# Kernel tuning notes

Hardware: AMD Instinct MI355X
Metric: run time of the kernel (lower is better)

## Reference

```python
import jax, jax.numpy as jnp
import numpy as np
import math

EMBED_DIM = 1024
N_HEAD = 16
HEAD_DIM = EMBED_DIM // N_HEAD


def setup_inputs() -> dict:
    key = jax.random.key(0)
    ks = jax.random.split(key, 9)
    B, T, C = 4, 2048, EMBED_DIM
    s = 1.0 / math.sqrt(C)
    return {
        "x": jax.random.normal(ks[0], (B, T, C), dtype=jnp.float32),
        "Wq": jax.random.normal(ks[1], (C, C), dtype=jnp.float32) * s,
        "bq": jnp.zeros((C,), dtype=jnp.float32),
        "Wk": jax.random.normal(ks[2], (C, C), dtype=jnp.float32) * s,
        "bk": jnp.zeros((C,), dtype=jnp.float32),
        "Wv": jax.random.normal(ks[3], (C, C), dtype=jnp.float32) * s,
        "bv": jnp.zeros((C,), dtype=jnp.float32),
        "Wp": jax.random.normal(ks[4], (C, C), dtype=jnp.float32) * s,
        "bp": jnp.zeros((C,), dtype=jnp.float32),
    }


def reference(x, Wq, bq, Wk, bk, Wv, bv, Wp, bp):
    B, T, C = x.shape
    H, D = N_HEAD, HEAD_DIM

    def heads(W, b):
        # [B,T,C] -> [B,H,T,D]
        return (x @ W.T + b).reshape(B, T, H, D).transpose(0, 2, 1, 3)

    q = heads(Wq, bq)
    k = heads(Wk, bk)
    v = heads(Wv, bv)

    att = jnp.einsum("bhtd,bhsd->bhts", q, k) * (1.0 / math.sqrt(D))
    causal = jnp.tril(jnp.ones((T, T), dtype=bool))
    att = jnp.where(causal[None, None], att, -jnp.inf)
    att = jax.nn.softmax(att, axis=-1)
    y = jnp.einsum("bhts,bhsd->bhtd", att, v)  # [B,H,T,D]
    y = y.transpose(0, 2, 1, 3).reshape(B, T, C)
    return y @ Wp.T + bp
```

## Files before the change

kernel.cpp:

```cpp
#include <hip/hip_runtime.h>
#include <hip/hip_bf16.h>
#include <cstdint>
#include <cstddef>

#define TQ 2048
#define CDIM 1024
#define NH 16
#define HD 64

typedef __attribute__((ext_vector_type(8))) short bf16x8;
typedef __attribute__((ext_vector_type(4))) float f32x4;
typedef __attribute__((ext_vector_type(16))) float f32x16;

__device__ __forceinline__ unsigned short f2bf(float f) {
  union { float f; unsigned u; } x; x.f = f;
  unsigned r = x.u + 0x7fffu + ((x.u >> 16) & 1u);
  return (unsigned short)(r >> 16);
}

__device__ __forceinline__ unsigned cvtpk(float lo, float hi) {
  unsigned r;
  asm("v_cvt_pk_bf16_f32 %0, %1, %2" : "=v"(r) : "v"(lo), "v"(hi));
  return r;
}

__device__ __forceinline__ void plswap(unsigned& x, unsigned& y) {
  asm("v_permlane32_swap_b32 %0, %1" : "+v"(x), "+v"(y));
}

__device__ __forceinline__ float exp2_fast(float x) {
  float r;
  asm("v_exp_f32 %0, %1" : "=v"(r) : "v"(x));
  return r;
}

__device__ __forceinline__ void gload_lds16(const void* g, void* l) {
  typedef __attribute__((address_space(1))) const void gv;
  typedef __attribute__((address_space(3))) void lv;
  __builtin_amdgcn_global_load_lds((gv*)g, (lv*)l, 16, 0, 0);
}

#define BAR() do { asm volatile("" ::: "memory"); __builtin_amdgcn_s_barrier(); asm volatile("" ::: "memory"); } while (0)
#define VMC2() asm volatile("s_waitcnt vmcnt(2)" ::: "memory")
#define VMC0() asm volatile("s_waitcnt vmcnt(0)" ::: "memory")

__global__ void cvt_bf16_kernel(const float* __restrict__ in,
                                unsigned short* __restrict__ out, int n) {
  int stride = gridDim.x * blockDim.x;
  for (int i = blockIdx.x * blockDim.x + threadIdx.x; i * 4 < n; i += stride) {
    float4 v = *(const float4*)(in + (size_t)i * 4);
    ushort4 o;
    o.x = f2bf(v.x); o.y = f2bf(v.y); o.z = f2bf(v.z); o.w = f2bf(v.w);
    *(ushort4*)(out + (size_t)i * 4) = o;
  }
}

__global__ void cvt4_kernel(const float* __restrict__ w0, const float* __restrict__ w1,
                            const float* __restrict__ w2, const float* __restrict__ w3,
                            unsigned short* __restrict__ out) {
  int i = blockIdx.x * blockDim.x + threadIdx.x;
  int which = i >> 18;
  const float* src = which == 0 ? w0 : which == 1 ? w1 : which == 2 ? w2 : w3;
  int off = (i & 262143) * 4;
  float4 v = *(const float4*)(src + off);
  ushort4 o;
  o.x = f2bf(v.x); o.y = f2bf(v.y); o.z = f2bf(v.z); o.w = f2bf(v.w);
  *(ushort4*)(out + (size_t)i * 4) = o;
}

template <int EPI>
__global__ __launch_bounds__(512, 2) void gemm128x256_kernel(
    const unsigned short* __restrict__ A,
    const unsigned short* __restrict__ Bt,
    const float* __restrict__ b0, const float* __restrict__ b1,
    void* __restrict__ outp,
    int M, int N, int K) {
  __shared__ __align__(16) char lds[98304];

  const int tid = (int)threadIdx.x;
  const int w = tid >> 6, lane = tid & 63;
  const int g = lane >> 4, c = lane & 15;
  const int wm = w >> 2, wn = w & 3;

  const int nbm = M >> 7, nbn = N >> 8;
  const int nwg = nbm * nbn;
  int id = (int)blockIdx.x;
  const int cpx = nwg >> 3;
  id = (id & 7) * cpx + (id >> 3);
  const int tm = id % nbm, tn = id / nbm;

  const char* Ab = (const char*)(A + (size_t)tm * 128 * K);
  const char* Bb = (const char*)(Bt + (size_t)tn * 256 * K);
  const int rowB = K * 2;
  const int nt = K >> 6;

  auto stageA = [&](int t) {
    if (t >= nt) return;
    char* dst = lds + (t & 1) * 49152 + (w << 11);
    const char* s = Ab + (size_t)(w * 16 + c) * rowB + t * 128 + g * 16;
    gload_lds16(s, dst);
    gload_lds16(s + 64, dst + 1024);
  };
  auto stageB = [&](int t, int odd) {
    if (t >= nt) return;
    const int n16 = (w >> 1) * 4 + 2 * odd + (w & 1);
    char* dst = lds + (t & 1) * 49152 + 16384 + (n16 << 11);
    const char* s = Bb + (size_t)(n16 * 16 + c) * rowB + t * 128 + g * 16;
    gload_lds16(s, dst);
    gload_lds16(s + 64, dst + 1024);
  };

  f32x4 acc[4][4];
#pragma unroll
  for (int i = 0; i < 4; ++i)
#pragma unroll
    for (int j = 0; j < 4; ++j) acc[i][j] = (f32x4){0.f, 0.f, 0.f, 0.f};
  bf16x8 af[2][2], bv[2][2][2];

  auto rdA = [&](int cur, int ms) {
#pragma unroll
    for (int mi2 = 0; mi2 < 2; ++mi2)
#pragma unroll
      for (int ki = 0; ki < 2; ++ki)
        af[mi2][ki] = *(const bf16x8*)(lds + cur * 49152 +
            (((wm * 4 + ms * 2 + mi2) << 1) + ki) * 1024 + lane * 16);
  };
  auto rdB = [&](int cur, int ns) {
#pragma unroll
    for (int ni2 = 0; ni2 < 2; ++ni2)
#pragma unroll
      for (int ki = 0; ki < 2; ++ki)
        bv[ns][ni2][ki] = *(const bf16x8*)(lds + cur * 49152 + 16384 +
            (((wn * 4 + ns * 2 + ni2) << 1) + ki) * 1024 + lane * 16);
  };
  auto mm = [&](int ms, int ns) {
    __builtin_amdgcn_s_setprio(1);
#pragma unroll
    for (int mi2 = 0; mi2 < 2; ++mi2)
#pragma unroll
      for (int ni2 = 0; ni2 < 2; ++ni2)
#pragma unroll
        for (int ki = 0; ki < 2; ++ki)
          acc[ms * 2 + mi2][ns * 2 + ni2] = __builtin_amdgcn_mfma_f32_16x16x32_bf16(
              af[mi2][ki], bv[ns][ni2][ki], acc[ms * 2 + mi2][ns * 2 + ni2], 0, 0, 0);
    __builtin_amdgcn_s_setprio(0);
  };

  stageA(0); stageB(0, 0); stageB(0, 1);
  VMC2();
  BAR();

#pragma unroll 1
  for (int i = 0; i < (nt >> 1); ++i) {
    const int t0 = 2 * i, t1 = 2 * i + 1;
    rdA(0, 0); rdB(0, 0); stageA(t0 + 1);
    mm(0, 0); VMC2(); BAR();
    rdB(0, 1); stageB(t0 + 1, 0);
    mm(0, 1); BAR();
    rdA(0, 1); stageB(t0 + 1, 1);
    mm(1, 1); BAR();
    mm(1, 0); VMC2(); BAR();
    rdA(1, 0); rdB(1, 0); stageA(t1 + 1);
    mm(0, 0);
    if (t1 == nt - 1) { VMC0(); } else { VMC2(); }
    BAR();
    rdB(1, 1); stageB(t1 + 1, 0);
    mm(0, 1); BAR();
    rdA(1, 1); stageB(t1 + 1, 1);
    mm(1, 1); BAR();
    mm(1, 0); VMC2(); BAR();
  }

#pragma unroll
  for (int mi = 0; mi < 4; ++mi) {
#pragma unroll
    for (int ni = 0; ni < 4; ++ni) {
      const int n = tn * 256 + wn * 64 + ni * 16 + c;
#pragma unroll
      for (int e = 0; e < 4; ++e) {
        const int m = tm * 128 + wm * 64 + mi * 16 + g * 4 + e;
        float v = acc[mi][ni][e];
        if (EPI == 1) {
          v += b0[m];
          size_t idx = ((size_t)(n >> 11) * (NH * HD) + m) * TQ + (n & (TQ - 1));
          ((unsigned short*)outp)[idx] = f2bf(v);
        } else if (EPI == 2) {
          v += b0[n];
          ((float*)outp)[(size_t)m * N + n] = v;
        } else {
          unsigned short* O = (unsigned short*)outp;
          if (n < 1024) {
            v = (v + b0[n]) * 0.18033688f;
            size_t idx = ((size_t)(m >> 11) * NH + (n >> 6)) * (TQ * HD) +
                         (size_t)(m & (TQ - 1)) * HD + (n & (HD - 1));
            O[idx] = f2bf(v);
          } else {
            int nn = n - 1024;
            v += b1[nn];
            size_t idx = 8388608 + ((size_t)(m >> 11) * NH + (nn >> 6)) * (TQ * HD) +
                         (size_t)(m & (TQ - 1)) * HD + (nn & (HD - 1));
            O[idx] = f2bf(v);
          }
        }
      }
    }
  }
}

__global__ __launch_bounds__(256, 4) void attn_kernel(
    const unsigned short* __restrict__ Q,
    const unsigned short* __restrict__ K,
    const unsigned short* __restrict__ Vt,
    unsigned short* __restrict__ Y) {
  __shared__ __align__(16) char Ks[2][8192];
  __shared__ __align__(16) char Vs[2][8192];

  const int tid = (int)threadIdx.x;
  const int w = tid >> 6, lane = tid & 63;
  const int l31 = lane & 31, hi = lane >> 5;

  const int n = (int)blockIdx.x;
  const int g = n & 255, k = n >> 8;
  const int bh = g >> 2;
  const int u = 2 * (g & 3) + (k >> 1);
  const int qt = (k & 1) ? (15 - u) : u;
  const int b = bh >> 4, h = bh & 15;

  const unsigned short* Qb = Q + (size_t)bh * TQ * HD;
  const char* Kb = (const char*)(K + (size_t)bh * TQ * HD);
  const char* Vb = (const char*)(Vt + (size_t)bh * HD * TQ);

  auto stage = [&](int buf, int kt) {
#pragma unroll
    for (int i = 0; i < 2; ++i) {
      const int s = i * 256 + tid;
      const int r32 = (s >> 8) * 32 + (s & 31);
      const int ck = ((s >> 6) & 3) * 32 + ((s >> 5) & 1) * 16;
      char* kdst = &Ks[buf][0] + i * 4096 + (w << 10);
      char* vdst = &Vs[buf][0] + i * 4096 + (w << 10);
      gload_lds16(Kb + (size_t)kt * 8192 + r32 * 128 + ck, kdst);
      gload_lds16(Vb + (size_t)r32 * 4096 + kt * 128 + ck, vdst);
    }
  };

  const int q0 = qt * 128 + w * 32;
  const int qg = q0 + l31;
  const int nkv = 2 * qt + 2;

  stage(0, 0);

  bf16x8 qf[4];
#pragma unroll
  for (int dk = 0; dk < 4; ++dk)
    qf[dk] = *(const bf16x8*)(Qb + (size_t)qg * HD + dk * 16 + hi * 8);

  f32x16 oac[2];
#pragma unroll
  for (int nb = 0; nb < 2; ++nb)
#pragma unroll
    for (int r = 0; r < 16; ++r) oac[nb][r] = 0.f;
  float mr = -3.0e38f, lr = 0.f;

  __syncthreads();

  for (int kt = 0; kt < nkv; ++kt) {
    const int cur = kt & 1;
    if (kt + 1 < nkv) stage(cur ^ 1, kt + 1);

    if (kt * 64 <= q0 + 31) {
      const char* Klane = &Ks[cur][0] + lane * 16;
      const char* Vlane = &Vs[cur][0] + lane * 16;

      f32x16 s0, s1;
#pragma unroll
      for (int r = 0; r < 16; ++r) { s0[r] = 0.f; s1[r] = 0.f; }
#pragma unroll
      for (int dk = 0; dk < 4; ++dk) {
        bf16x8 kf0 = *(const bf16x8*)(Klane + (dk << 10));
        bf16x8 kf1 = *(const bf16x8*)(Klane + ((4 + dk) << 10));
        s0 = __builtin_amdgcn_mfma_f32_32x32x16_bf16(kf0, qf[dk], s0, 0, 0, 0);
        s1 = __builtin_amdgcn_mfma_f32_32x32x16_bf16(kf1, qf[dk], s1, 0, 0, 0);
      }

      const bool maskT = (kt * 64 + 63 > q0);
      if (maskT) {
#pragma unroll
        for (int r = 0; r < 16; ++r) {
          int kv0 = kt * 64 + ((r & 3) + 8 * (r >> 2)) + 4 * hi;
          s0[r] = (kv0 <= qg) ? s0[r] : -3.0e38f;
          s1[r] = (kv0 + 32 <= qg) ? s1[r] : -3.0e38f;
        }
      }

      float mt_ = s0[0];
#pragma unroll
      for (int r = 1; r < 16; ++r) mt_ = fmaxf(mt_, s0[r]);
#pragma unroll
      for (int r = 0; r < 16; ++r) mt_ = fmaxf(mt_, s1[r]);
      mt_ = fmaxf(mt_, __shfl_xor(mt_, 32));

      if (!__all(mt_ - mr <= 8.0f)) {
        const float mn = fmaxf(mr, mt_);
        const float al = exp2_fast(mr - mn);
        mr = mn;
        lr *= al;
#pragma unroll
        for (int nb = 0; nb < 2; ++nb)
#pragma unroll
          for (int r = 0; r < 16; ++r) oac[nb][r] *= al;
      }

      float rs = 0.f;
#pragma unroll
      for (int r = 0; r < 16; ++r) { s0[r] = exp2_fast(s0[r] - mr); rs += s0[r]; }
#pragma unroll
      for (int r = 0; r < 16; ++r) { s1[r] = exp2_fast(s1[r] - mr); rs += s1[r]; }
      rs += __shfl_xor(rs, 32);
      lr += rs;

      bf16x8 pf[4];
      {
        unsigned a0 = cvtpk(s0[0], s0[1]), b0 = cvtpk(s0[2], s0[3]);
        unsigned c0 = cvtpk(s0[4], s0[5]), d0 = cvtpk(s0[6], s0[7]);
        plswap(a0, c0); plswap(b0, d0);
        unsigned a1 = cvtpk(s0[8], s0[9]), b1 = cvtpk(s0[10], s0[11]);
        unsigned c1 = cvtpk(s0[12], s0[13]), d1 = cvtpk(s0[14], s0[15]);
        plswap(a1, c1); plswap(b1, d1);
        unsigned a2 = cvtpk(s1[0], s1[1]), b2 = cvtpk(s1[2], s1[3]);
        unsigned c2 = cvtpk(s1[4], s1[5]), d2 = cvtpk(s1[6], s1[7]);
        plswap(a2, c2); plswap(b2, d2);
        unsigned a3 = cvtpk(s1[8], s1[9]), b3 = cvtpk(s1[10], s1[11]);
        unsigned c3 = cvtpk(s1[12], s1[13]), d3 = cvtpk(s1[14], s1[15]);
        plswap(a3, c3); plswap(b3, d3);
        union { unsigned u[4]; bf16x8 v; } t;
        t.u[0] = a0; t.u[1] = b0; t.u[2] = c0; t.u[3] = d0; pf[0] = t.v;
        t.u[0] = a1; t.u[1] = b1; t.u[2] = c1; t.u[3] = d1; pf[1] = t.v;
        t.u[0] = a2; t.u[1] = b2; t.u[2] = c2; t.u[3] = d2; pf[2] = t.v;
        t.u[0] = a3; t.u[1] = b3; t.u[2] = c3; t.u[3] = d3; pf[3] = t.v;
      }

#pragma unroll
      for (int nb = 0; nb < 2; ++nb)
#pragma unroll
        for (int ks = 0; ks < 4; ++ks) {
          bf16x8 vf = *(const bf16x8*)(Vlane + (((nb << 2) + ks) << 10));
          oac[nb] = __builtin_amdgcn_mfma_f32_32x32x16_bf16(vf, pf[ks], oac[nb], 0, 0, 0);
        }
    }
    __syncthreads();
  }

  float inv;
  asm("v_rcp_f32 %0, %1" : "=v"(inv) : "v"(lr));
  unsigned short* Yrow = Y + (size_t)(b * TQ + qg) * CDIM + h * 64;
#pragma unroll
  for (int nb = 0; nb < 2; ++nb)
#pragma unroll
    for (int j = 0; j < 8; ++j) {
      const int dbase = ((2 * j) & 3) + 8 * (j >> 1);
      unsigned lo = f2bf(oac[nb][2 * j] * inv);
      unsigned hi2 = f2bf(oac[nb][2 * j + 1] * inv);
      *(unsigned*)(Yrow + nb * 32 + dbase + 4 * hi) = lo | (hi2 << 16);
    }
}

extern "C" void kernel_launch(void* const* d_in, const int* in_sizes, int n_in,
                              void* d_out, int out_size, void* d_ws, size_t ws_size,
                              hipStream_t stream) {
  (void)in_sizes; (void)n_in; (void)out_size; (void)ws_size;
  const float* x  = (const float*)d_in[0];
  const float* Wq = (const float*)d_in[1];
  const float* bq = (const float*)d_in[2];
  const float* Wk = (const float*)d_in[3];
  const float* bk = (const float*)d_in[4];
  const float* Wv = (const float*)d_in[5];
  const float* bv = (const float*)d_in[6];
  const float* Wp = (const float*)d_in[7];
  const float* bp = (const float*)d_in[8];
  float* out = (float*)d_out;

  char* ws = (char*)d_ws;
  unsigned short* xb  = (unsigned short*)(ws + 0);
  unsigned short* wqb = (unsigned short*)(ws + 16777216);
  unsigned short* wvb = (unsigned short*)(ws + 20971520);
  unsigned short* wpb = (unsigned short*)(ws + 23068672);
  unsigned short* Qh  = (unsigned short*)(ws + 25165824);
  unsigned short* Kh  = (unsigned short*)(ws + 41943040);
  unsigned short* Vt  = (unsigned short*)(ws + 58720256);
  unsigned short* y   = (unsigned short*)(ws + 75497472);

  const int nx = 4 * TQ * CDIM;

  cvt_bf16_kernel<<<4096, 256, 0, stream>>>(x, xb, nx);
  cvt4_kernel<<<4096, 256, 0, stream>>>(Wq, Wk, Wv, Wp, wqb);

  gemm128x256_kernel<4><<<512, 512, 0, stream>>>(xb, wqb, bq, bk, Qh, 8192, 2048, 1024);
  gemm128x256_kernel<1><<<256, 512, 0, stream>>>(wvb, xb, bv, bv, Vt, 1024, 8192, 1024);

  attn_kernel<<<1024, 256, 0, stream>>>(Qh, Kh, Vt, y);

  gemm128x256_kernel<2><<<256, 512, 0, stream>>>(y, wpb, bp, bp, out, 8192, 1024, 1024);
}
```

Before: 209.4 us.

## Add 256x256 tile GEMM with 8-phase pipelined LDS schedule for QK projection

Introduces a new GEMM kernel with 256x256 output tiles, 128KB of LDS double buffering, and an interleaved schedule that overlaps LDS reads, async global-to-LDS stages and MFMA phases. It is used for the fused Q/K projection, halving the block count and raising data reuse per tile. Separately, the attention kernel's launch bounds are raised to 5 waves per SIMD, which limits registers per thread. The larger LDS footprint lowers occupancy and leaves 256 blocks, which may underfill the CUs.

Result: no change. 212.3 us (+1.4%).

```diff
diff --git a/kernel.cpp b/kernel.cpp
--- a/kernel.cpp
+++ b/kernel.cpp
@@ -66,6 +66,137 @@
   ushort4 o;
   o.x = f2bf(v.x); o.y = f2bf(v.y); o.z = f2bf(v.z); o.w = f2bf(v.w);
   *(ushort4*)(out + (size_t)i * 4) = o;
+}
+
+template <int EPI>
+__global__ __launch_bounds__(512, 2) void gemm256_kernel(
+    const unsigned short* __restrict__ A,
+    const unsigned short* __restrict__ Bt,
+    const float* __restrict__ b0, const float* __restrict__ b1,
+    void* __restrict__ outp,
+    int M, int N, int K) {
+  __shared__ __align__(16) char lds[131072];
+
+  const int tid = (int)threadIdx.x;
+  const int w = tid >> 6, lane = tid & 63;
+  const int g = lane >> 4, c = lane & 15;
+  const int wm = w >> 2, wn = w & 3;
+
+  const int nbm = M >> 8, nbn = N >> 8;
+  const int nwg = nbm * nbn;
+  int id = (int)blockIdx.x;
+  const int cpx = nwg >> 3;
+  id = (id & 7) * cpx + (id >> 3);
+  const int tm = id % nbm, tn = id / nbm;
+
+  const char* Ab = (const char*)(A + (size_t)tm * 256 * K);
+  const char* Bb = (const char*)(Bt + (size_t)tn * 256 * K);
+  const int rowB = K * 2;
+  const int nht = (K >> 6) << 2;
+
+  char* aw = lds + wm * 16384;
+  char* bw = lds + 65536 + (wn >> 1) * 16384;
+  const int bfo = (wn & 1) * 8;
+
+  auto stage_ht = [&](int j) {
+    if (j >= nht) return;
+    const int t = j >> 2, part = j & 3;
+    const int isB = part >> 1, half = part & 1;
+    const char* src = isB ? Bb : Ab;
+    char* dst = lds + isB * 65536 + (t & 1) * 32768 + half * 16384 + w * 2048;
+#pragma unroll
+    for (int r = 0; r < 2; ++r) {
+      const int f = w * 2 + r;
+      const int m16 = f >> 1, ki = f & 1;
+      gload_lds16(src + (size_t)(half * 128 + m16 * 16 + c) * rowB +
+                      t * 128 + ki * 64 + g * 16,
+                  dst + r * 1024);
+    }
+  };
+
+  f32x4 acc[8][4];
+#pragma unroll
+  for (int i = 0; i < 8; ++i)
+#pragma unroll
+    for (int j = 0; j < 4; ++j) acc[i][j] = (f32x4){0.f, 0.f, 0.f, 0.f};
+  bf16x8 af[4][2], bv[2][2];
+
+  auto rdA = [&](int buf, int ms) {
+#pragma unroll
+    for (int mi = 0; mi < 4; ++mi)
+#pragma unroll
+      for (int ki = 0; ki < 2; ++ki)
+        af[mi][ki] = *(const bf16x8*)(aw + buf * 32768 +
+                                      ((ms * 4 + mi) * 2 + ki) * 1024 + lane * 16);
+  };
+  auto rdB = [&](int buf, int ns) {
+#pragma unroll
+    for (int ni = 0; ni < 2; ++ni)
+#pragma unroll
+      for (int ki = 0; ki < 2; ++ki)
+        bv[ni][ki] = *(const bf16x8*)(bw + buf * 32768 +
+                                      (bfo + (ns * 2 + ni) * 2 + ki) * 1024 + lane * 16);
+  };
+  auto mm = [&](int ms, int ns) {
+    __builtin_amdgcn_s_setprio(1);
+#pragma unroll
+    for (int mi = 0; mi < 4; ++mi)
+#pragma unroll
+      for (int ni = 0; ni < 2; ++ni)
+#pragma unroll
+        for (int ki = 0; ki < 2; ++ki)
+          acc[ms * 4 + mi][ns * 2 + ni] = __builtin_amdgcn_mfma_f32_16x16x32_bf16(
+              af[mi][ki], bv[ni][ki], acc[ms * 4 + mi][ns * 2 + ni], 0, 0, 0);
+    __builtin_amdgcn_s_setprio(0);
+  };
+
+  for (int j = 0; j < 5; ++j) stage_ht(j);
+  VMC2();
+  BAR();
+
+  const int niter = K >> 7;
+#pragma unroll 1
+  for (int i = 0; i < niter; ++i) {
+    const int j0 = 5 + (i << 3);
+    rdA(0, 0); rdB(0, 0); stage_ht(j0 + 0); BAR(); mm(0, 0); BAR();
+    rdB(0, 1);            stage_ht(j0 + 1); BAR(); mm(0, 1); BAR();
+    rdA(0, 1);            stage_ht(j0 + 2); BAR(); mm(1, 1); BAR();
+    rdB(0, 0);            stage_ht(j0 + 3);
+    if (i + 1 < niter) { VMC2(); } else { VMC0(); }
+    BAR(); mm(1, 0); BAR();
+    rdA(1, 0); rdB(1, 0); stage_ht(j0 + 4); BAR(); mm(0, 0); BAR();
+    rdB(1, 1);            stage_ht(j0 + 5); BAR(); mm(0, 1); BAR();
+    rdA(1, 1);            stage_ht(j0 + 6); BAR(); mm(1, 1); BAR();
+    rdB(1, 0);            stage_ht(j0 + 7); VMC2(); BAR(); mm(1, 0); BAR();
+  }
+
+#pragma unroll
+  for (int mi = 0; mi < 8; ++mi) {
+#pragma unroll
+    for (int ni = 0; ni < 4; ++ni) {
+      const int n = tn * 256 + wn * 64 + ni * 16 + c;
+#pragma unroll
+      for (int e = 0; e < 4; ++e) {
+        const int m = tm * 256 + wm * 128 + mi * 16 + g * 4 + e;
+        float v = acc[mi][ni][e];
+        if (EPI == 4) {
+          unsigned short* O = (unsigned short*)outp;
+          if (n < 1024) {
+            v = (v + b0[n]) * 0.18033688f;
+            size_t idx = ((size_t)(m >> 11) * NH + (n >> 6)) * (TQ * HD) +
+                         (size_t)(m & (TQ - 1)) * HD + (n & (HD - 1));
+            O[idx] = f2bf(v);
+          } else {
+            int nn = n - 1024;
+            v += b1[nn];
+            size_t idx = 8388608 + ((size_t)(m >> 11) * NH + (nn >> 6)) * (TQ * HD) +
+                         (size_t)(m & (TQ - 1)) * HD + (nn & (HD - 1));
+            O[idx] = f2bf(v);
+          }
+        }
+      }
+    }
+  }
 }
 
 template <int EPI>
@@ -187,27 +318,13 @@
         } else if (EPI == 2) {
           v += b0[n];
           ((float*)outp)[(size_t)m * N + n] = v;
-        } else {
-          unsigned short* O = (unsigned short*)outp;
-          if (n < 1024) {
-            v = (v + b0[n]) * 0.18033688f;
-            size_t idx = ((size_t)(m >> 11) * NH + (n >> 6)) * (TQ * HD) +
-                         (size_t)(m & (TQ - 1)) * HD + (n & (HD - 1));
-            O[idx] = f2bf(v);
-          } else {
-            int nn = n - 1024;
-            v += b1[nn];
-            size_t idx = 8388608 + ((size_t)(m >> 11) * NH + (nn >> 6)) * (TQ * HD) +
-                         (size_t)(m & (TQ - 1)) * HD + (nn & (HD - 1));
-            O[idx] = f2bf(v);
-          }
         }
       }
     }
   }
 }
 
-__global__ __launch_bounds__(256, 4) void attn_kernel(
+__global__ __launch_bounds__(256, 5) void attn_kernel(
     const unsigned short* __restrict__ Q,
     const unsigned short* __restrict__ K,
     const unsigned short* __restrict__ Vt,
@@ -394,7 +511,7 @@
   cvt_bf16_kernel<<<4096, 256, 0, stream>>>(x, xb, nx);
   cvt4_kernel<<<4096, 256, 0, stream>>>(Wq, Wk, Wv, Wp, wqb);
 
-  gemm128x256_kernel<4><<<512, 512, 0, stream>>>(xb, wqb, bq, bk, Qh, 8192, 2048, 1024);
+  gemm256_kernel<4><<<256, 512, 0, stream>>>(xb, wqb, bq, bk, Qh, 8192, 2048, 1024);
   gemm128x256_kernel<1><<<256, 512, 0, stream>>>(wvb, xb, bv, bv, Vt, 1024, 8192, 1024);
 
   attn_kernel<<<1024, 256, 0, stream>>>(Qh, Kh, Vt, y);
```
